# Kernel optimization log

Hardware: AMD Instinct MI355X
Metric: run time of the kernel (lower is better)

## Reference

```python
import jax, jax.numpy as jnp
import numpy as np
import math

D_MODEL = 1024
N_HEADS = 16
D_KV = 64
INNER = N_HEADS * D_KV
D_FF = 4096
NUM_BUCKETS = 32
MAX_DIST = 128
EPS = 1e-6
B, S = 2, 1024


def _t5_layernorm(x, w):
    # T5 RMSNorm: no mean subtraction, no bias
    var = jnp.mean(x * x, axis=-1, keepdims=True)
    return x * jax.lax.rsqrt(var + EPS) * w


def _relative_position_bucket(relative_position):
    # bidirectional (encoder) variant of T5 bucketing
    num_buckets = NUM_BUCKETS // 2
    rel_buckets = (relative_position > 0).astype(jnp.int32) * num_buckets
    rp = jnp.abs(relative_position)
    max_exact = num_buckets // 2
    is_small = rp < max_exact
    rp_large = max_exact + (
        jnp.log(rp.astype(jnp.float32) / max_exact)
        / math.log(MAX_DIST / max_exact)
        * (num_buckets - max_exact)
    ).astype(jnp.int32)
    rp_large = jnp.minimum(rp_large, num_buckets - 1)
    return rel_buckets + jnp.where(is_small, rp, rp_large)


def setup_inputs() -> dict:
    key = jax.random.key(0)
    ks = jax.random.split(key, 8)
    sc = 0.02
    return {
        "hidden_states": jax.random.normal(ks[0], (B, S, D_MODEL), jnp.float32),
        "ln1_w": jnp.ones((D_MODEL,), jnp.float32),
        "wq": jax.random.normal(ks[1], (INNER, D_MODEL), jnp.float32) * sc,
        "wk": jax.random.normal(ks[2], (INNER, D_MODEL), jnp.float32) * sc,
        "wv": jax.random.normal(ks[3], (INNER, D_MODEL), jnp.float32) * sc,
        "wo": jax.random.normal(ks[4], (D_MODEL, INNER), jnp.float32) * sc,
        "rel_bias": jax.random.normal(ks[5], (NUM_BUCKETS, N_HEADS), jnp.float32) * sc,
        "ln2_w": jnp.ones((D_MODEL,), jnp.float32),
        "wi": jax.random.normal(ks[6], (D_FF, D_MODEL), jnp.float32) * sc,
        "wo_ff": jax.random.normal(ks[7], (D_MODEL, D_FF), jnp.float32) * sc,
    }


def reference(hidden_states, ln1_w, wq, wk, wv, wo, rel_bias, ln2_w, wi, wo_ff):
    b, s, _ = hidden_states.shape
    # --- self-attention with relative position bias (T5: no 1/sqrt(d) scale) ---
    x = _t5_layernorm(hidden_states, ln1_w)
    q = (x @ wq.T).reshape(b, s, N_HEADS, D_KV).transpose(0, 2, 1, 3)  # [b,h,s,d]
    k = (x @ wk.T).reshape(b, s, N_HEADS, D_KV).transpose(0, 2, 1, 3)
    v = (x @ wv.T).reshape(b, s, N_HEADS, D_KV).transpose(0, 2, 1, 3)
    pos = jnp.arange(s)
    buckets = _relative_position_bucket(pos[None, :] - pos[:, None])  # [s,s]
    bias = rel_bias[buckets].transpose(2, 0, 1)[None]  # [1,h,s,s]
    scores = jnp.einsum('bhqd,bhkd->bhqk', q, k) + bias
    attn = jax.nn.softmax(scores, axis=-1)
    ctx = jnp.einsum('bhqk,bhkd->bhqd', attn, v)
    ctx = ctx.transpose(0, 2, 1, 3).reshape(b, s, INNER)
    h = hidden_states + ctx @ wo.T
    # --- FFN (ReLU dense) with pre-norm and residual ---
    y = _t5_layernorm(h, ln2_w)
    ff = jax.nn.relu(y @ wi.T) @ wo_ff.T
    return h + ff
```

## Files before the change

kernel.cpp:

```cpp
#include <hip/hip_runtime.h>
#include <hip/hip_bf16.h>
#include <math.h>


typedef __bf16 bf16_t;
typedef __attribute__((ext_vector_type(8))) __bf16 bf16x8;
typedef __attribute__((ext_vector_type(4))) __bf16 bf16x4;
typedef __attribute__((ext_vector_type(4))) float floatx4;

#define GLOBAL_AS(p) ((const __attribute__((address_space(1))) void*)(p))
#define LDS_AS(p)    ((__attribute__((address_space(3))) void*)(p))

__global__ __launch_bounds__(256) void convert_w_kernel(
    const float* __restrict__ wq, const float* __restrict__ wk,
    const float* __restrict__ wv, const float* __restrict__ wo,
    const float* __restrict__ wi, const float* __restrict__ woff,
    bf16_t* __restrict__ wqkv_b, bf16_t* __restrict__ wo_b,
    bf16_t* __restrict__ wi_b, bf16_t* __restrict__ woff_b) {
  size_t idx = ((size_t)blockIdx.x * 256 + threadIdx.x) * 8;
  const float* src;
  bf16_t* dst;
  size_t off;
  if (idx < 3145728) {
    size_t sec = idx >> 20;
    src = sec == 0 ? wq : (sec == 1 ? wk : wv);
    dst = wqkv_b + (sec << 20);
    off = idx & 1048575;
  } else if (idx < 4194304) {
    src = wo; dst = wo_b; off = idx - 3145728;
  } else if (idx < 8388608) {
    src = wi; dst = wi_b; off = idx - 4194304;
  } else {
    src = woff; dst = woff_b; off = idx - 8388608;
  }
  float4 a = *(const float4*)(src + off);
  float4 b = *(const float4*)(src + off + 4);
  bf16x8 o;
  o[0] = (bf16_t)a.x; o[1] = (bf16_t)a.y; o[2] = (bf16_t)a.z; o[3] = (bf16_t)a.w;
  o[4] = (bf16_t)b.x; o[5] = (bf16_t)b.y; o[6] = (bf16_t)b.z; o[7] = (bf16_t)b.w;
  *(bf16x8*)(dst + off) = o;
}

__global__ __launch_bounds__(256) void prologue_kernel(
    const float* __restrict__ hs, const float* __restrict__ ln1w,
    const float* __restrict__ rel_bias, bf16_t* __restrict__ x,
    float* __restrict__ table) {
  int bid = blockIdx.x;
  int t = threadIdx.x;
  if (bid < 2048) {
    const int D = 1024;
    float4 v = ((const float4*)(hs + (size_t)bid * D))[t];
    float f[4] = {v.x, v.y, v.z, v.w};
    float s = 0.f;
#pragma unroll
    for (int j = 0; j < 4; ++j) s += f[j] * f[j];
#pragma unroll
    for (int off = 32; off > 0; off >>= 1) s += __shfl_down(s, off);
    __shared__ float red[4];
    int lane = t & 63, wave = t >> 6;
    if (lane == 0) red[wave] = s;
    __syncthreads();
    float tot = red[0] + red[1] + red[2] + red[3];
    float scale = rsqrtf(tot * (1.0f / D) + 1e-6f);
    float4 wv4 = ((const float4*)ln1w)[t];
    bf16x4 o;
    o[0] = (bf16_t)(f[0] * scale * wv4.x);
    o[1] = (bf16_t)(f[1] * scale * wv4.y);
    o[2] = (bf16_t)(f[2] * scale * wv4.z);
    o[3] = (bf16_t)(f[3] * scale * wv4.w);
    *(bf16x4*)(x + (size_t)bid * D + t * 4) = o;
  } else {
    int idx = (bid - 2048) * 256 + t;
    int h = idx >> 11;
    int dpos = idx & 2047;
    int delta = dpos - 1023;
    if (delta > 1023) delta = 1023;
    int side = (delta > 0) ? 16 : 0;
    int rp = (delta < 0) ? -delta : delta;
    int bucket;
    if (rp < 8) {
      bucket = side + rp;
    } else {
      float t3 = (logf((float)rp * 0.125f) / 2.7725887f) * 8.0f;
      int v = 8 + (int)t3;
      if (v > 15) v = 15;
      bucket = side + v;
    }
    table[idx] = rel_bias[bucket * 16 + h];
  }
}

template <int TBM, bool WF32, int OP>
__global__ __launch_bounds__(256, 3) void gemm_bt(
    const bf16_t* __restrict__ A, const void* __restrict__ W0,
    const void* __restrict__ W1, const void* __restrict__ W2,
    bf16_t* __restrict__ C, int M, int K_total, int klen, int N,
    int wsel_cols) {
  constexpr int MFRAG = TBM / 32;
  __shared__ bf16_t As[TBM * 64];
  __shared__ bf16_t Bs[128 * 64];

  const int tid = threadIdx.x;
  const int lane = tid & 63;
  const int wv = tid >> 6;
  const int wm = wv & 1;
  const int wn = wv >> 1;
  const int lr = lane & 15;
  const int lq = lane >> 4;

  int bx = blockIdx.x, by = blockIdx.y;
  {
    int gx = gridDim.x, gy = gridDim.y;
    int lid = by * gx + bx;
    int xcd = lid & 7, slot = lid >> 3;
    int per = gy >> 3;
    by = xcd * per + slot % per;
    bx = slot / per;
  }

  const size_t row0 = (size_t)bx * TBM;
  const size_t col0 = (size_t)by * 128;
  const int k0 = blockIdx.z * klen;

  const void* Ws = W0;
  size_t wc0 = col0;
  if ((int)col0 >= wsel_cols) {
    if ((int)col0 < 2 * wsel_cols) { Ws = W1; wc0 = col0 - wsel_cols; }
    else { Ws = W2; wc0 = col0 - 2 * (size_t)wsel_cols; }
  }

  const bf16_t* Abase = A + row0 * K_total;
  bf16_t* Cs = C + (size_t)blockIdx.z * M * N;

  floatx4 acc[MFRAG][4] = {};

  for (int kt = k0; kt < k0 + klen; kt += 64) {
#pragma unroll
    for (int i = 0; i < TBM / 32; ++i) {
      int chunk = i * 256 + tid;
      int r = chunk >> 3;
      int kc = ((chunk & 7) ^ (r & 7)) << 3;
      __builtin_amdgcn_global_load_lds(
          GLOBAL_AS(Abase + (size_t)r * K_total + kt + kc),
          LDS_AS(As + (size_t)(i * 256 + wv * 64) * 8), 16, 0, 0);
    }
    if constexpr (WF32) {
      const float* Wbase = (const float*)Ws + wc0 * K_total;
#pragma unroll
      for (int i = 0; i < 4; ++i) {
        int chunk = i * 256 + tid;
        int r = chunk >> 3;
        int kc = ((chunk & 7) ^ (r & 7)) << 3;
        const float* p = Wbase + (size_t)r * K_total + kt + kc;
        float4 f0 = *(const float4*)p;
        float4 f1v = *(const float4*)(p + 4);
        bf16x8 o;
        o[0] = (bf16_t)f0.x; o[1] = (bf16_t)f0.y;
        o[2] = (bf16_t)f0.z; o[3] = (bf16_t)f0.w;
        o[4] = (bf16_t)f1v.x; o[5] = (bf16_t)f1v.y;
        o[6] = (bf16_t)f1v.z; o[7] = (bf16_t)f1v.w;
        *(bf16x8*)(Bs + chunk * 8) = o;
      }
    } else {
      const bf16_t* Wbase = (const bf16_t*)Ws + wc0 * K_total;
#pragma unroll
      for (int i = 0; i < 4; ++i) {
        int chunk = i * 256 + tid;
        int r = chunk >> 3;
        int kc = ((chunk & 7) ^ (r & 7)) << 3;
        __builtin_amdgcn_global_load_lds(
            GLOBAL_AS(Wbase + (size_t)r * K_total + kt + kc),
            LDS_AS(Bs + (size_t)(i * 256 + wv * 64) * 8), 16, 0, 0);
      }
    }
    __syncthreads();

#pragma unroll
    for (int c = 0; c < 2; ++c) {
      bf16x8 af[MFRAG], bfr[4];
#pragma unroll
      for (int mi = 0; mi < MFRAG; ++mi) {
        int rr = wm * (TBM / 2) + mi * 16 + lr;
        int c8p = (c * 4 + lq) ^ (rr & 7);
        af[mi] = *(const bf16x8*)(As + rr * 64 + c8p * 8);
      }
#pragma unroll
      for (int nj = 0; nj < 4; ++nj) {
        int rr = wn * 64 + nj * 16 + lr;
        int c8p = (c * 4 + lq) ^ (rr & 7);
        bfr[nj] = *(const bf16x8*)(Bs + rr * 64 + c8p * 8);
      }
#pragma unroll
      for (int mi = 0; mi < MFRAG; ++mi)
#pragma unroll
        for (int nj = 0; nj < 4; ++nj)
          acc[mi][nj] = __builtin_amdgcn_mfma_f32_16x16x32_bf16(
              af[mi], bfr[nj], acc[mi][nj], 0, 0, 0);
    }
    __syncthreads();
  }

#pragma unroll
  for (int mi = 0; mi < MFRAG; ++mi) {
#pragma unroll
    for (int nj = 0; nj < 4; ++nj) {
      size_t r = row0 + wm * (TBM / 2) + mi * 16 + lq * 4;
      size_t c = col0 + wn * 64 + nj * 16 + lr;
#pragma unroll
      for (int t = 0; t < 4; ++t) {
        float v = acc[mi][nj][t];
        if (OP == 2) v = v > 0.f ? v : 0.f;
        Cs[(r + t) * N + c] = (bf16_t)v;
      }
    }
  }
}

__global__ __launch_bounds__(256) void transpose_v_kernel(
    const bf16_t* __restrict__ QKV, bf16_t* __restrict__ VT) {
  __shared__ bf16_t T[64 * 65];
  const int s0 = blockIdx.x * 64;
  const int h = blockIdx.y;
  const int b = blockIdx.z;
  const int tid = threadIdx.x;

  const bf16_t* Vh = QKV + ((size_t)b * 1024) * 3072 + 2048 + h * 64;
#pragma unroll
  for (int i = 0; i < 2; ++i) {
    int c = i * 256 + tid;
    int r = c >> 3;
    int d8 = (c & 7) * 8;
    bf16x8 v = *(const bf16x8*)(Vh + (size_t)(s0 + r) * 3072 + d8);
#pragma unroll
    for (int j = 0; j < 8; ++j) T[r * 65 + d8 + j] = v[j];
  }
  __syncthreads();

  bf16_t* Og = VT + ((size_t)b * 16 + h) * 64 * 1024;
#pragma unroll
  for (int i = 0; i < 2; ++i) {
    int c = i * 256 + tid;
    int d = c >> 3;
    int s8 = (c & 7) * 8;
    bf16x8 o;
#pragma unroll
    for (int j = 0; j < 8; ++j) o[j] = T[(s8 + j) * 65 + d];
    *(bf16x8*)(Og + (size_t)d * 1024 + s0 + s8) = o;
  }
}

__device__ __forceinline__ void attn_stage(const bf16_t* Kh, const bf16_t* Vg,
                                           int k0, bf16_t* Ksb, bf16_t* Vtb,
                                           int tid, int wv) {
  const int l16 = tid & 15;
  const int lo8 = ((tid & 63) >> 4) * 8;
#pragma unroll
  for (int i = 0; i < 2; ++i) {
    int bi = wv * 2 + i;
    int g = bi >> 1, c = bi & 1;
    __builtin_amdgcn_global_load_lds(
        GLOBAL_AS(Kh + (size_t)(k0 + g * 16 + l16) * 3072 + c * 32 + lo8),
        LDS_AS(Ksb + bi * 512), 16, 0, 0);
    __builtin_amdgcn_global_load_lds(
        GLOBAL_AS(Vg + (size_t)(g * 16 + l16) * 1024 + k0 + c * 32 + lo8),
        LDS_AS(Vtb + bi * 512), 16, 0, 0);
  }
}

__global__ __launch_bounds__(256) void attn_kernel(
    const bf16_t* __restrict__ QKV, const bf16_t* __restrict__ VT,
    const float* __restrict__ bias_table, bf16_t* __restrict__ O) {
  const int qt = blockIdx.x;
  const int h = blockIdx.y;
  const int b = blockIdx.z;
  const int tid = threadIdx.x;
  const int lane = tid & 63;
  const int wv = tid >> 6;
  const int lr = lane & 15;
  const int lq = lane >> 4;

  __shared__ bf16_t Ks[2][4096];
  __shared__ bf16_t Vt[2][4096];
  __shared__ bf16_t Ps[4][1024];

  const bf16_t* Qh = QKV + (size_t)b * 1024 * 3072 + h * 64;
  const bf16_t* Kh = Qh + 1024;
  const bf16_t* Vg = VT + ((size_t)b * 16 + h) * 64 * 1024;
  bf16_t* Oh = O + (size_t)b * 1024 * 1024 + h * 64;

  const int q0w = qt * 64 + wv * 16;
  const int myq = q0w + lr;

  bf16x8 qf[2];
#pragma unroll
  for (int c = 0; c < 2; ++c)
    qf[c] = *(const bf16x8*)(Qh + (size_t)(q0w + lr) * 3072 + c * 32 + lq * 8);

  float l_loc = 0.f;
  floatx4 o_acc[4];
#pragma unroll
  for (int i = 0; i < 4; ++i) o_acc[i] = (floatx4){0.f, 0.f, 0.f, 0.f};

  const float* btab = bias_table + h * 2048 + 1023 - myq;

  attn_stage(Kh, Vg, 0, Ks[0], Vt[0], tid, wv);
  __syncthreads();

  for (int kt = 0; kt < 16; ++kt) {
    const int k0 = kt * 64;
    if (kt < 15)
      attn_stage(Kh, Vg, k0 + 64, Ks[(kt + 1) & 1], Vt[(kt + 1) & 1], tid, wv);
    const bf16_t* Ksb = Ks[kt & 1];
    const bf16_t* Vtb = Vt[kt & 1];

    floatx4 s_acc[4];
#pragma unroll
    for (int g = 0; g < 4; ++g) {
      floatx4 a = (floatx4){0.f, 0.f, 0.f, 0.f};
#pragma unroll
      for (int c = 0; c < 2; ++c) {
        bf16x8 kf = *(const bf16x8*)(Ksb + (g * 2 + c) * 512 + lane * 8);
        a = __builtin_amdgcn_mfma_f32_16x16x32_bf16(kf, qf[c], a, 0, 0, 0);
      }
      s_acc[g] = a;
    }

#pragma unroll
    for (int g = 0; g < 4; ++g) {
      bf16x4 pb;
#pragma unroll
      for (int t = 0; t < 4; ++t) {
        int key = k0 + g * 16 + lq * 4 + t;
        float p = __expf(s_acc[g][t] + btab[key] - 32.0f);
        l_loc += p;
        pb[t] = (bf16_t)p;
      }
      int c = g >> 1;
      int dst = c * 512 + (((g & 1) * 2 + (lq >> 1)) * 16 + lr) * 8 + (lq & 1) * 4;
      *(bf16x4*)(&Ps[wv][dst]) = pb;
    }

    asm volatile("s_waitcnt lgkmcnt(0)" ::: "memory");

    bf16x8 pf[2];
#pragma unroll
    for (int c = 0; c < 2; ++c)
      pf[c] = *(const bf16x8*)(&Ps[wv][c * 512 + lane * 8]);

#pragma unroll
    for (int g = 0; g < 4; ++g) {
#pragma unroll
      for (int c = 0; c < 2; ++c) {
        bf16x8 vf = *(const bf16x8*)(Vtb + (g * 2 + c) * 512 + lane * 8);
        o_acc[g] = __builtin_amdgcn_mfma_f32_16x16x32_bf16(pf[c], vf, o_acc[g], 0, 0, 0);
      }
    }
    __syncthreads();
  }

  l_loc += __shfl_xor(l_loc, 16);
  l_loc += __shfl_xor(l_loc, 32);
  float inv = 1.f / l_loc;

  float invt[4];
#pragma unroll
  for (int t = 0; t < 4; ++t) invt[t] = __shfl(inv, lq * 4 + t);

#pragma unroll
  for (int g = 0; g < 4; ++g) {
#pragma unroll
    for (int t = 0; t < 4; ++t) {
      int qg = q0w + lq * 4 + t;
      int d = g * 16 + lr;
      Oh[(size_t)qg * 1024 + d] = (bf16_t)(o_acc[g][t] * invt[t]);
    }
  }
}

__global__ __launch_bounds__(256) void reduce_rms_kernel(
    const bf16_t* __restrict__ part, int splits, const float* __restrict__ hs,
    const float* __restrict__ ln2w, bf16_t* __restrict__ hbuf,
    bf16_t* __restrict__ y) {
  const size_t SLICE = (size_t)2048 * 1024;
  int tid = threadIdx.x;
  size_t i = ((size_t)blockIdx.x * 256 + tid) * 8;

  float s[8] = {};
  for (int sp = 0; sp < splits; ++sp) {
    bf16x8 p = *(const bf16x8*)(part + sp * SLICE + i);
#pragma unroll
    for (int j = 0; j < 8; ++j) s[j] += (float)p[j];
  }
  float4 a = *(const float4*)(hs + i);
  float4 b = *(const float4*)(hs + i + 4);
  s[0] += a.x; s[1] += a.y; s[2] += a.z; s[3] += a.w;
  s[4] += b.x; s[5] += b.y; s[6] += b.z; s[7] += b.w;

  bf16x8 hb;
#pragma unroll
  for (int j = 0; j < 8; ++j) hb[j] = (bf16_t)s[j];
  *(bf16x8*)(hbuf + i) = hb;

  float ss = 0.f;
#pragma unroll
  for (int j = 0; j < 8; ++j) ss += s[j] * s[j];
#pragma unroll
  for (int off = 32; off > 0; off >>= 1) ss += __shfl_down(ss, off);
  __shared__ float red[4];
  int wave = tid >> 6;
  if ((tid & 63) == 0) red[wave] = ss;
  __syncthreads();
  float rowss = (tid < 128) ? (red[0] + red[1]) : (red[2] + red[3]);
  float scale = rsqrtf(rowss * (1.f / 1024.f) + 1e-6f);

  int col = (int)(i & 1023);
  float4 w0 = *(const float4*)(ln2w + col);
  float4 w1 = *(const float4*)(ln2w + col + 4);
  bf16x8 o;
  o[0] = (bf16_t)(s[0] * scale * w0.x); o[1] = (bf16_t)(s[1] * scale * w0.y);
  o[2] = (bf16_t)(s[2] * scale * w0.z); o[3] = (bf16_t)(s[3] * scale * w0.w);
  o[4] = (bf16_t)(s[4] * scale * w1.x); o[5] = (bf16_t)(s[5] * scale * w1.y);
  o[6] = (bf16_t)(s[6] * scale * w1.z); o[7] = (bf16_t)(s[7] * scale * w1.w);
  *(bf16x8*)(y + i) = o;
}

__global__ __launch_bounds__(256) void reduce_out_kernel(
    const bf16_t* __restrict__ part, int splits,
    const bf16_t* __restrict__ res, float* __restrict__ out) {
  const size_t SLICE = (size_t)2048 * 1024;
  size_t i = ((size_t)blockIdx.x * 256 + threadIdx.x) * 8;
  float s[8] = {};
  for (int sp = 0; sp < splits; ++sp) {
    bf16x8 p = *(const bf16x8*)(part + sp * SLICE + i);
#pragma unroll
    for (int j = 0; j < 8; ++j) s[j] += (float)p[j];
  }
  bf16x8 r = *(const bf16x8*)(res + i);
#pragma unroll
  for (int j = 0; j < 8; ++j) s[j] += (float)r[j];
  float4 a, b;
  a.x = s[0]; a.y = s[1]; a.z = s[2]; a.w = s[3];
  b.x = s[4]; b.y = s[5]; b.z = s[6]; b.w = s[7];
  *(float4*)(out + i) = a;
  *(float4*)(out + i + 4) = b;
}

extern "C" void kernel_launch(void* const* d_in, const int* in_sizes, int n_in,
                              void* d_out, int out_size, void* d_ws,
                              size_t ws_size, hipStream_t stream) {
  const float* hs = (const float*)d_in[0];
  const float* ln1_w = (const float*)d_in[1];
  const float* wq = (const float*)d_in[2];
  const float* wk = (const float*)d_in[3];
  const float* wvv = (const float*)d_in[4];
  const float* wo = (const float*)d_in[5];
  const float* rel_bias = (const float*)d_in[6];
  const float* ln2_w = (const float*)d_in[7];
  const float* wi = (const float*)d_in[8];
  const float* wo_ff = (const float*)d_in[9];
  float* out = (float*)d_out;

  const int M = 2048, D = 1024, FF = 4096;
  const size_t SL = (size_t)M * D * 2;
  const size_t QKVB = (size_t)M * 3072 * 2;
  const size_t F1B = (size_t)M * FF * 2;
  const size_t BT = 16 * 2048 * 4;

  const size_t FULL_NEED = BT + 6291456 + 2097152 + 8388608 + 8388608 +
                           SL + QKVB + SL + SL + SL + F1B + SL + 4 * SL;
  const size_t COMPACT_NEED = BT + SL + QKVB + F1B;

  char* w = (char*)d_ws;
  dim3 gtv(16, 16, 2), ga(16, 16, 2);

  if (ws_size >= FULL_NEED) {
    float* btab = (float*)w;      w += BT;
    bf16_t* wqkv_b = (bf16_t*)w;  w += 6291456;
    bf16_t* wo_b = (bf16_t*)w;    w += 2097152;
    bf16_t* wi_b = (bf16_t*)w;    w += 8388608;
    bf16_t* woff_b = (bf16_t*)w;  w += 8388608;
    bf16_t* x = (bf16_t*)w;       w += SL;
    bf16_t* qkv = (bf16_t*)w;     w += QKVB;
    bf16_t* ctx = (bf16_t*)w;     w += SL;
    bf16_t* hbuf = (bf16_t*)w;    w += SL;
    bf16_t* y = (bf16_t*)w;       w += SL;
    bf16_t* f1 = (bf16_t*)w;      w += F1B;
    bf16_t* vtg = (bf16_t*)w;     w += SL;
    bf16_t* part = (bf16_t*)w;    w += 4 * SL;

    convert_w_kernel<<<6144, 256, 0, stream>>>(wq, wk, wvv, wo, wi, wo_ff,
                                               wqkv_b, wo_b, wi_b, woff_b);
    prologue_kernel<<<2176, 256, 0, stream>>>(hs, ln1_w, rel_bias, x, btab);

    gemm_bt<128, false, 0><<<dim3(16, 24, 1), 256, 0, stream>>>(
        x, wqkv_b, wqkv_b, wqkv_b, qkv, M, D, D, 3072, 1 << 30);
    transpose_v_kernel<<<gtv, 256, 0, stream>>>(qkv, vtg);
    attn_kernel<<<ga, 256, 0, stream>>>(qkv, vtg, btab, ctx);

    gemm_bt<128, false, 0><<<dim3(16, 8, 4), 256, 0, stream>>>(
        ctx, wo_b, wo_b, wo_b, part, M, D, D / 4, D, 1 << 30);
    reduce_rms_kernel<<<1024, 256, 0, stream>>>(part, 4, hs, ln2_w, hbuf, y);

    gemm_bt<128, false, 2><<<dim3(16, 32, 1), 256, 0, stream>>>(
        y, wi_b, wi_b, wi_b, f1, M, D, D, FF, 1 << 30);

    gemm_bt<128, false, 0><<<dim3(16, 8, 4), 256, 0, stream>>>(
        f1, woff_b, woff_b, woff_b, part, M, FF, FF / 4, D, 1 << 30);
    reduce_out_kernel<<<1024, 256, 0, stream>>>(part, 4, hbuf, out);
  } else {
    if (ws_size < COMPACT_NEED) return;
    float* btab = (float*)w;  w += BT;
    char* Abuf = w;           w += SL;
    char* Bbuf = w;           w += QKVB;
    char* Fbuf = w;           w += F1B;
    bf16_t* x = (bf16_t*)Abuf;
    bf16_t* ctx = (bf16_t*)Abuf;
    bf16_t* hbuf = (bf16_t*)Abuf;
    bf16_t* qkv = (bf16_t*)Bbuf;
    bf16_t* part = (bf16_t*)Bbuf;
    bf16_t* y = (bf16_t*)(Bbuf + 2 * SL);
    bf16_t* vtg = (bf16_t*)Fbuf;
    bf16_t* f1 = (bf16_t*)Fbuf;

    prologue_kernel<<<2176, 256, 0, stream>>>(hs, ln1_w, rel_bias, x, btab);

    gemm_bt<64, true, 0><<<dim3(32, 24, 1), 256, 0, stream>>>(
        x, wq, wk, wvv, qkv, M, D, D, 3072, 1024);
    transpose_v_kernel<<<gtv, 256, 0, stream>>>(qkv, vtg);
    attn_kernel<<<ga, 256, 0, stream>>>(qkv, vtg, btab, ctx);

    gemm_bt<64, true, 0><<<dim3(32, 8, 2), 256, 0, stream>>>(
        ctx, wo, wo, wo, part, M, D, D / 2, D, 1 << 30);
    reduce_rms_kernel<<<1024, 256, 0, stream>>>(part, 2, hs, ln2_w, hbuf, y);

    gemm_bt<64, true, 2><<<dim3(32, 32, 1), 256, 0, stream>>>(
        y, wi, wi, wi, f1, M, D, D, FF, 1 << 30);

    gemm_bt<64, true, 0><<<dim3(32, 8, 2), 256, 0, stream>>>(
        f1, wo_ff, wo_ff, wo_ff, part, M, FF, FF / 2, D, 1 << 30);
    reduce_out_kernel<<<1024, 256, 0, stream>>>(part, 2, hbuf, out);
  }
}
```

Before: 233.0 us.

## Fuse weight conversion into prologue, V-transpose into QKV GEMM epilogue, stage stores via LDS

```diff
diff --git a/kernel.cpp b/kernel.cpp
--- a/kernel.cpp
+++ b/kernel.cpp
@@ -11,45 +11,45 @@
 #define GLOBAL_AS(p) ((const __attribute__((address_space(1))) void*)(p))
 #define LDS_AS(p)    ((__attribute__((address_space(3))) void*)(p))
 
-__global__ __launch_bounds__(256) void convert_w_kernel(
-    const float* __restrict__ wq, const float* __restrict__ wk,
-    const float* __restrict__ wv, const float* __restrict__ wo,
-    const float* __restrict__ wi, const float* __restrict__ woff,
-    bf16_t* __restrict__ wqkv_b, bf16_t* __restrict__ wo_b,
-    bf16_t* __restrict__ wi_b, bf16_t* __restrict__ woff_b) {
-  size_t idx = ((size_t)blockIdx.x * 256 + threadIdx.x) * 8;
-  const float* src;
-  bf16_t* dst;
-  size_t off;
-  if (idx < 3145728) {
-    size_t sec = idx >> 20;
-    src = sec == 0 ? wq : (sec == 1 ? wk : wv);
-    dst = wqkv_b + (sec << 20);
-    off = idx & 1048575;
-  } else if (idx < 4194304) {
-    src = wo; dst = wo_b; off = idx - 3145728;
-  } else if (idx < 8388608) {
-    src = wi; dst = wi_b; off = idx - 4194304;
-  } else {
-    src = woff; dst = woff_b; off = idx - 8388608;
-  }
-  float4 a = *(const float4*)(src + off);
-  float4 b = *(const float4*)(src + off + 4);
-  bf16x8 o;
-  o[0] = (bf16_t)a.x; o[1] = (bf16_t)a.y; o[2] = (bf16_t)a.z; o[3] = (bf16_t)a.w;
-  o[4] = (bf16_t)b.x; o[5] = (bf16_t)b.y; o[6] = (bf16_t)b.z; o[7] = (bf16_t)b.w;
-  *(bf16x8*)(dst + off) = o;
-}
-
 __global__ __launch_bounds__(256) void prologue_kernel(
     const float* __restrict__ hs, const float* __restrict__ ln1w,
-    const float* __restrict__ rel_bias, bf16_t* __restrict__ x,
-    float* __restrict__ table) {
+    const float* __restrict__ rel_bias, const float* __restrict__ wq,
+    const float* __restrict__ wk, const float* __restrict__ wv,
+    const float* __restrict__ wo, const float* __restrict__ wi,
+    const float* __restrict__ woff, bf16_t* __restrict__ x,
+    float* __restrict__ table, bf16_t* __restrict__ wqkv_b,
+    bf16_t* __restrict__ wo_b, bf16_t* __restrict__ wi_b,
+    bf16_t* __restrict__ woff_b, int do_convert) {
   int bid = blockIdx.x;
   int t = threadIdx.x;
-  if (bid < 2048) {
+  if (bid < 6144) {
+    if (!do_convert) return;
+    size_t idx = ((size_t)bid * 256 + t) * 8;
+    const float* src;
+    bf16_t* dst;
+    size_t off;
+    if (idx < 3145728) {
+      size_t sec = idx >> 20;
+      src = sec == 0 ? wq : (sec == 1 ? wk : wv);
+      dst = wqkv_b + (sec << 20);
+      off = idx & 1048575;
+    } else if (idx < 4194304) {
+      src = wo; dst = wo_b; off = idx - 3145728;
+    } else if (idx < 8388608) {
+      src = wi; dst = wi_b; off = idx - 4194304;
+    } else {
+      src = woff; dst = woff_b; off = idx - 8388608;
+    }
+    float4 a = *(const float4*)(src + off);
+    float4 b = *(const float4*)(src + off + 4);
+    bf16x8 o;
+    o[0] = (bf16_t)a.x; o[1] = (bf16_t)a.y; o[2] = (bf16_t)a.z; o[3] = (bf16_t)a.w;
+    o[4] = (bf16_t)b.x; o[5] = (bf16_t)b.y; o[6] = (bf16_t)b.z; o[7] = (bf16_t)b.w;
+    *(bf16x8*)(dst + off) = o;
+  } else if (bid < 8192) {
+    int row = bid - 6144;
     const int D = 1024;
-    float4 v = ((const float4*)(hs + (size_t)bid * D))[t];
+    float4 v = ((const float4*)(hs + (size_t)row * D))[t];
     float f[4] = {v.x, v.y, v.z, v.w};
     float s = 0.f;
 #pragma unroll
@@ -68,9 +68,9 @@
     o[1] = (bf16_t)(f[1] * scale * wv4.y);
     o[2] = (bf16_t)(f[2] * scale * wv4.z);
     o[3] = (bf16_t)(f[3] * scale * wv4.w);
-    *(bf16x4*)(x + (size_t)bid * D + t * 4) = o;
+    *(bf16x4*)(x + (size_t)row * D + t * 4) = o;
   } else {
-    int idx = (bid - 2048) * 256 + t;
+    int idx = (bid - 8192) * 256 + t;
     int h = idx >> 11;
     int dpos = idx & 2047;
     int delta = dpos - 1023;
@@ -94,11 +94,13 @@
 __global__ __launch_bounds__(256, 3) void gemm_bt(
     const bf16_t* __restrict__ A, const void* __restrict__ W0,
     const void* __restrict__ W1, const void* __restrict__ W2,
-    bf16_t* __restrict__ C, int M, int K_total, int klen, int N,
-    int wsel_cols) {
+    bf16_t* __restrict__ C, bf16_t* __restrict__ VT, int M, int K_total,
+    int klen, int N, int wsel_cols, int vtsel) {
   constexpr int MFRAG = TBM / 32;
-  __shared__ bf16_t As[TBM * 64];
-  __shared__ bf16_t Bs[128 * 64];
+  constexpr int WROWS = TBM / 2;
+  __shared__ bf16_t buf[(TBM + 128) * 64];
+  bf16_t* As = buf;
+  bf16_t* Bs = buf + TBM * 64;
 
   const int tid = threadIdx.x;
   const int lane = tid & 63;
@@ -180,7 +182,7 @@
       bf16x8 af[MFRAG], bfr[4];
 #pragma unroll
       for (int mi = 0; mi < MFRAG; ++mi) {
-        int rr = wm * (TBM / 2) + mi * 16 + lr;
+        int rr = wm * WROWS + mi * 16 + lr;
         int c8p = (c * 4 + lq) ^ (rr & 7);
         af[mi] = *(const bf16x8*)(As + rr * 64 + c8p * 8);
       }
@@ -200,18 +202,44 @@
     __syncthreads();
   }
 
-#pragma unroll
-  for (int mi = 0; mi < MFRAG; ++mi) {
-#pragma unroll
-    for (int nj = 0; nj < 4; ++nj) {
-      size_t r = row0 + wm * (TBM / 2) + mi * 16 + lq * 4;
-      size_t c = col0 + wn * 64 + nj * 16 + lr;
-#pragma unroll
-      for (int t = 0; t < 4; ++t) {
-        float v = acc[mi][nj][t];
-        if (OP == 2) v = v > 0.f ? v : 0.f;
-        Cs[(r + t) * N + c] = (bf16_t)v;
-      }
+  if ((int)col0 >= vtsel) {
+    int b = (int)(row0 >> 10);
+#pragma unroll
+    for (int mi = 0; mi < MFRAG; ++mi) {
+#pragma unroll
+      for (int nj = 0; nj < 4; ++nj) {
+        int d = (int)col0 - 2048 + wn * 64 + nj * 16 + lr;
+        int h = d >> 6, dd = d & 63;
+        int r = (int)row0 + wm * WROWS + mi * 16 + lq * 4;
+        int s = r & 1023;
+        bf16x4 pv;
+#pragma unroll
+        for (int t = 0; t < 4; ++t) pv[t] = (bf16_t)acc[mi][nj][t];
+        *(bf16x4*)(VT + (((size_t)b * 16 + h) * 64 + dd) * 1024 + s) = pv;
+      }
+    }
+  } else {
+    bf16_t* wbuf = buf + wv * (WROWS * 64);
+#pragma unroll
+    for (int mi = 0; mi < MFRAG; ++mi) {
+#pragma unroll
+      for (int nj = 0; nj < 4; ++nj) {
+#pragma unroll
+        for (int t = 0; t < 4; ++t) {
+          float v = acc[mi][nj][t];
+          if (OP == 2) v = v > 0.f ? v : 0.f;
+          wbuf[(mi * 16 + lq * 4 + t) * 64 + nj * 16 + lr] = (bf16_t)v;
+        }
+      }
+    }
+    asm volatile("s_waitcnt lgkmcnt(0)" ::: "memory");
+#pragma unroll
+    for (int p = 0; p < WROWS / 8; ++p) {
+      int i = p * 8 + (lane >> 3);
+      int cc = (lane & 7) * 8;
+      bf16x8 vvv = *(const bf16x8*)(wbuf + i * 64 + cc);
+      size_t gr = row0 + wm * WROWS + i;
+      *(bf16x8*)(Cs + gr * N + col0 + wn * 64 + cc) = vvv;
     }
   }
 }
@@ -465,13 +493,14 @@
   const size_t QKVB = (size_t)M * 3072 * 2;
   const size_t F1B = (size_t)M * FF * 2;
   const size_t BT = 16 * 2048 * 4;
+  const int NOVT = 1 << 30;
 
   const size_t FULL_NEED = BT + 6291456 + 2097152 + 8388608 + 8388608 +
                            SL + QKVB + SL + SL + SL + F1B + SL + 4 * SL;
   const size_t COMPACT_NEED = BT + SL + QKVB + F1B;
 
   char* w = (char*)d_ws;
-  dim3 gtv(16, 16, 2), ga(16, 16, 2);
+  dim3 ga(16, 16, 2);
 
   if (ws_size >= FULL_NEED) {
     float* btab = (float*)w;      w += BT;
@@ -488,24 +517,24 @@
     bf16_t* vtg = (bf16_t*)w;     w += SL;
     bf16_t* part = (bf16_t*)w;    w += 4 * SL;
 
-    convert_w_kernel<<<6144, 256, 0, stream>>>(wq, wk, wvv, wo, wi, wo_ff,
-                                               wqkv_b, wo_b, wi_b, woff_b);
-    prologue_kernel<<<2176, 256, 0, stream>>>(hs, ln1_w, rel_bias, x, btab);
+    prologue_kernel<<<8320, 256, 0, stream>>>(
+        hs, ln1_w, rel_bias, wq, wk, wvv, wo, wi, wo_ff, x, btab, wqkv_b,
+        wo_b, wi_b, woff_b, 1);
 
     gemm_bt<128, false, 0><<<dim3(16, 24, 1), 256, 0, stream>>>(
-        x, wqkv_b, wqkv_b, wqkv_b, qkv, M, D, D, 3072, 1 << 30);
-    transpose_v_kernel<<<gtv, 256, 0, stream>>>(qkv, vtg);
+        x, wqkv_b, wqkv_b, wqkv_b, qkv, vtg, M, D, D, 3072, NOVT, 2048);
     attn_kernel<<<ga, 256, 0, stream>>>(qkv, vtg, btab, ctx);
 
     gemm_bt<128, false, 0><<<dim3(16, 8, 4), 256, 0, stream>>>(
-        ctx, wo_b, wo_b, wo_b, part, M, D, D / 4, D, 1 << 30);
+        ctx, wo_b, wo_b, wo_b, part, nullptr, M, D, D / 4, D, NOVT, NOVT);
     reduce_rms_kernel<<<1024, 256, 0, stream>>>(part, 4, hs, ln2_w, hbuf, y);
 
     gemm_bt<128, false, 2><<<dim3(16, 32, 1), 256, 0, stream>>>(
-        y, wi_b, wi_b, wi_b, f1, M, D, D, FF, 1 << 30);
+        y, wi_b, wi_b, wi_b, f1, nullptr, M, D, D, FF, NOVT, NOVT);
 
     gemm_bt<128, false, 0><<<dim3(16, 8, 4), 256, 0, stream>>>(
-        f1, woff_b, woff_b, woff_b, part, M, FF, FF / 4, D, 1 << 30);
+        f1, woff_b, woff_b, woff_b, part, nullptr, M, FF, FF / 4, D, NOVT,
+        NOVT);
     reduce_out_kernel<<<1024, 256, 0, stream>>>(part, 4, hbuf, out);
   } else {
     if (ws_size < COMPACT_NEED) return;
@@ -522,22 +551,25 @@
     bf16_t* vtg = (bf16_t*)Fbuf;
     bf16_t* f1 = (bf16_t*)Fbuf;
 
-    prologue_kernel<<<2176, 256, 0, stream>>>(hs, ln1_w, rel_bias, x, btab);
+    prologue_kernel<<<8320, 256, 0, stream>>>(
+        hs, ln1_w, rel_bias, wq, wk, wvv, wo, wi, wo_ff, x, btab, nullptr,
+        nullptr, nullptr, nullptr, 0);
 
     gemm_bt<64, true, 0><<<dim3(32, 24, 1), 256, 0, stream>>>(
-        x, wq, wk, wvv, qkv, M, D, D, 3072, 1024);
-    transpose_v_kernel<<<gtv, 256, 0, stream>>>(qkv, vtg);
+        x, wq, wk, wvv, qkv, nullptr, M, D, D, 3072, 1024, NOVT);
+    transpose_v_kernel<<<dim3(16, 16, 2), 256, 0, stream>>>(qkv, vtg);
     attn_kernel<<<ga, 256, 0, stream>>>(qkv, vtg, btab, ctx);
 
     gemm_bt<64, true, 0><<<dim3(32, 8, 2), 256, 0, stream>>>(
-        ctx, wo, wo, wo, part, M, D, D / 2, D, 1 << 30);
+        ctx, wo, wo, wo, part, nullptr, M, D, D / 2, D, NOVT, NOVT);
     reduce_rms_kernel<<<1024, 256, 0, stream>>>(part, 2, hs, ln2_w, hbuf, y);
 
     gemm_bt<64, true, 2><<<dim3(32, 32, 1), 256, 0, stream>>>(
-        y, wi, wi, wi, f1, M, D, D, FF, 1 << 30);
+        y, wi, wi, wi, f1, nullptr, M, D, D, FF, NOVT, NOVT);
 
     gemm_bt<64, true, 0><<<dim3(32, 8, 2), 256, 0, stream>>>(
-        f1, wo_ff, wo_ff, wo_ff, part, M, FF, FF / 2, D, 1 << 30);
+        f1, wo_ff, wo_ff, wo_ff, part, nullptr, M, FF, FF / 2, D, NOVT,
+        NOVT);
     reduce_out_kernel<<<1024, 256, 0, stream>>>(part, 2, hbuf, out);
   }
 }
```

After: 228.5 us. No clear change (-1.9%).
